# Optimization experiments

Measured on AMD Instinct MI355X. Metric: run time of the kernel, lower is better.

Reference implementation:

```python
import jax, jax.numpy as jnp
import numpy as np

B = 32
L = 256
NUM_AA = 20
LAMBDA_SINGLE = 1.0
LAMBDA_PAIR = 0.2 * (L - 1)


def setup_inputs() -> dict:
    key = jax.random.key(0)
    k1, k2, k3 = jax.random.split(key, 3)
    x = jax.random.randint(k1, (B, L), 0, NUM_AA, dtype=jnp.int32)
    # Embedding(num, 1) init: normal(0, embedding_dim**-0.5) = std 1.0
    w_single = jax.random.normal(k2, (L * NUM_AA, 1), dtype=jnp.float32)
    w_pair = jax.random.normal(k3, (L * L * NUM_AA * NUM_AA, 1), dtype=jnp.float32)
    return {"x": x, "w_single": w_single, "w_pair": w_pair}


def reference(x, w_single, w_pair):
    ws = w_single[:, 0]  # [L*20]
    wp = w_pair[:, 0]    # [L*L*400]
    Bn, Ln = x.shape
    pos = jnp.arange(Ln, dtype=jnp.int32)

    # singles[b, i] = ws[i*20 + x[b, i]]
    singles = ws[pos[None, :] * NUM_AA + x]  # [B, L]
    all_singles = jnp.broadcast_to(ws.reshape(Ln, NUM_AA), (Bn, Ln, NUM_AA))  # [B, L, 20]

    # pairs[b, i, j] = wp[(i*L + j)*400 + x[b,i]*20 + x[b,j]]
    idx_pairs = (pos[:, None] * Ln + pos[None, :]) * (NUM_AA * NUM_AA) \
        + x[:, :, None] * NUM_AA + x[:, None, :]  # [B, L, L]
    pairs = wp[idx_pairs]  # [B, L, L]

    # all_pairs reproduces the original in-place mutation semantics:
    # at outer iteration i (inner loop over j), x[:, p] has already been
    # overwritten to 19 for p < i, equals j for p == i, and is original for p > i.
    i_ax = pos[None, :, None, None]                      # [1, L, 1, 1]
    p_ax = pos[None, None, :, None]                      # [1, 1, L, 1]
    j_ax = jnp.arange(NUM_AA, dtype=jnp.int32)[None, None, None, :]  # [1,1,1,20]
    x_b = x[:, None, :, None]                            # [B, 1, L, 1]
    eff = jnp.where(p_ax < i_ax, NUM_AA - 1, jnp.where(p_ax == i_ax, j_ax, x_b))
    idx_all = (i_ax * Ln + p_ax) * (NUM_AA * NUM_AA) + j_ax * NUM_AA + eff  # [B,L,L,20]
    all_pairs = wp[idx_all]  # [B, L, L, 20]

    energy = singles + jnp.sum(pairs, axis=2)  # [B, L]
    logits = all_singles + jnp.sum(all_pairs, axis=2)  # [B, L, 20]
    total_energy = jax.nn.logsumexp(logits, axis=-1)  # [B, L]
    final_energy = jnp.mean(jnp.sum(-energy + total_energy, axis=1))

    single_reg = LAMBDA_SINGLE * jnp.sum(jnp.square(w_single))
    pair_reg = LAMBDA_PAIR * jnp.sum(jnp.square(w_pair))
    single_lasso = LAMBDA_SINGLE * jnp.sum(jnp.abs(w_single))
    pair_lasso = LAMBDA_PAIR * jnp.sum(jnp.abs(w_pair))
    return final_energy + single_reg + pair_reg + single_lasso + pair_lasso
```

## Files before the change

### kernel.cpp

```cpp
#include <hip/hip_runtime.h>
#include <cmath>

#define Bsz 32
#define Lsz 256
#define Asz 20
#define PAD 21
#define NCHUNK 4
#define PCH 64
#define GRP 8
#define NGRP (PCH/GRP)
#define BLK1 640

#define OFF_G 0
#define OFF_C (NCHUNK*Bsz*Lsz*Asz)
#define OFF_E (OFF_C + NCHUNK*Lsz*Asz)
#define OFF_RSQ (OFF_E + NCHUNK*Bsz*Lsz)
#define OFF_RAB (OFF_RSQ + Lsz*NCHUNK)
#define OFF_K2  (OFF_RAB + Lsz*NCHUNK)

__global__ __launch_bounds__(BLK1) void k1(const int* __restrict__ x,
                                           const float* __restrict__ wp,
                                           float* __restrict__ ws) {
  const int wg = blockIdx.x;
  const int c = wg & (NCHUNK - 1);
  const int i = wg >> 2;
  const int t = threadIdx.x;
  const int b = t / Asz;
  const int j = t - b * Asz;

  __shared__ float blk[GRP * Asz * PAD];
  __shared__ int   xs[Bsz * PCH];
  __shared__ int   xi[Bsz];
  __shared__ float red1[BLK1];
  __shared__ float red2[BLK1];

  const int pbase = c * PCH;
  for (int k = t; k < Bsz * PCH; k += BLK1) {
    int bb = k >> 6, pp = k & 63;
    xs[k] = x[bb * Lsz + pbase + pp];
  }
  if (t < Bsz) xi[t] = x[t * Lsz + i];
  __syncthreads();

  float accJ = 0.f;
  float accE = 0.f;
  float accC = 0.f;
  float rsq = 0.f, rab = 0.f;

  const float* wrow = wp + (size_t)(i * Lsz + pbase) * (Asz * Asz);

  float v0, v1, v2, v3, v4;
  {
    const float* g0 = wrow;
    v0 = g0[t]; v1 = g0[t + BLK1]; v2 = g0[t + 2*BLK1];
    v3 = g0[t + 3*BLK1]; v4 = g0[t + 4*BLK1];
  }

  for (int g = 0; g < NGRP; ++g) {
    {
      float vv[5] = {v0, v1, v2, v3, v4};
      #pragma unroll
      for (int k = 0; k < 5; ++k) {
        float v = vv[k];
        rsq += v * v;
        rab += fabsf(v);
        int o = k * BLK1 + t;
        int bi = o / 400;
        int w = o - bi * 400;
        int r = w / 20;
        int col = w - r * 20;
        blk[bi * (Asz * PAD) + r * PAD + col] = v;
      }
    }
    __syncthreads();

    if (g + 1 < NGRP) {
      const float* ns = wrow + (g + 1) * (GRP * 400);
      v0 = ns[t]; v1 = ns[t + BLK1]; v2 = ns[t + 2*BLK1];
      v3 = ns[t + 3*BLK1]; v4 = ns[t + 4*BLK1];
    }

    const int p0 = pbase + g * GRP;
    #pragma unroll
    for (int pp = 0; pp < GRP; ++pp) {
      const int p = p0 + pp;
      const float* bb = blk + pp * (Asz * PAD);
      const int xv = xs[b * PCH + (p - pbase)];
      if (p > i) accJ += bb[j * PAD + xv];
      if (j == 0) accE += bb[xi[b] * PAD + xv];
      if (t < Asz) {
        if (p < i)       accC += bb[t * PAD + 19];
        else if (p == i) accC += bb[t * PAD + t];
      }
    }
    __syncthreads();
  }

  ws[OFF_G + (((size_t)c * Bsz + b) * Lsz + i) * Asz + j] = accJ;
  if (j == 0) ws[OFF_E + (c * Bsz + b) * Lsz + i] = accE;
  if (t < Asz) ws[OFF_C + (c * Lsz + i) * Asz + t] = accC;

  red1[t] = rsq; red2[t] = rab;
  __syncthreads();
  for (int s = 320; s >= 5; s >>= 1) {
    if (t < s) { red1[t] += red1[t + s]; red2[t] += red2[t + s]; }
    __syncthreads();
  }
  if (t == 0) {
    ws[OFF_RSQ + wg] = red1[0] + red1[1] + red1[2] + red1[3] + red1[4];
    ws[OFF_RAB + wg] = red2[0] + red2[1] + red2[2] + red2[3] + red2[4];
  }
}

__global__ __launch_bounds__(256) void k2(const int* __restrict__ x,
                                          const float* __restrict__ wsingle,
                                          const float* __restrict__ ws,
                                          float* __restrict__ wso) {
  const int t = threadIdx.x;
  const int row = blockIdx.x * 256 + t;
  const int b = row >> 8;
  const int i = row & 255;

  float logits[Asz];
  float m = -1e30f;
  #pragma unroll
  for (int j = 0; j < Asz; ++j) {
    float v = wsingle[i * Asz + j];
    #pragma unroll
    for (int c = 0; c < NCHUNK; ++c) {
      v += ws[OFF_C + (c * Lsz + i) * Asz + j];
      v += ws[OFF_G + (((size_t)c * Bsz + b) * Lsz + i) * Asz + j];
    }
    logits[j] = v;
    m = fmaxf(m, v);
  }
  float se = 0.f;
  #pragma unroll
  for (int j = 0; j < Asz; ++j) se += expf(logits[j] - m);
  float lse = m + logf(se);

  float en = wsingle[i * Asz + x[b * Lsz + i]];
  #pragma unroll
  for (int c = 0; c < NCHUNK; ++c) en += ws[OFF_E + (c * Bsz + b) * Lsz + i];

  float val = lse - en;
  __shared__ float red[256];
  red[t] = val;
  __syncthreads();
  for (int s = 128; s >= 1; s >>= 1) {
    if (t < s) red[t] += red[t + s];
    __syncthreads();
  }
  if (t == 0) wso[OFF_K2 + blockIdx.x] = red[0];
}

__global__ __launch_bounds__(256) void k3(const float* __restrict__ wsingle,
                                          const float* __restrict__ ws,
                                          float* __restrict__ out) {
  const int t = threadIdx.x;
  float ssq = 0.f, sab = 0.f;
  for (int k = t; k < Lsz * Asz; k += 256) {
    float v = wsingle[k];
    ssq += v * v; sab += fabsf(v);
  }
  float psq = 0.f, pab = 0.f;
  for (int k = t; k < Lsz * NCHUNK; k += 256) {
    psq += ws[OFF_RSQ + k];
    pab += ws[OFF_RAB + k];
  }
  float fe = 0.f;
  if (t < 32) fe = ws[OFF_K2 + t];

  const float LP = (float)(0.2 * 255.0);
  float val = fe * (1.0f / Bsz) + (ssq + sab) + LP * (psq + pab);

  __shared__ float red[256];
  red[t] = val;
  __syncthreads();
  for (int s = 128; s >= 1; s >>= 1) {
    if (t < s) red[t] += red[t + s];
    __syncthreads();
  }
  if (t == 0) out[0] = red[0];
}

extern "C" void kernel_launch(void* const* d_in, const int* in_sizes, int n_in,
                              void* d_out, int out_size, void* d_ws, size_t ws_size,
                              hipStream_t stream) {
  const int*   x       = (const int*)d_in[0];
  const float* wsingle = (const float*)d_in[1];
  const float* wpair   = (const float*)d_in[2];
  float* ws  = (float*)d_ws;
  float* out = (float*)d_out;

  k1<<<Lsz * NCHUNK, BLK1, 0, stream>>>(x, wpair, ws);
  k2<<<(Bsz * Lsz) / 256, 256, 0, stream>>>(x, wsingle, ws, ws);
  k3<<<1, 256, 0, stream>>>(wsingle, ws, out);
}
```

Baseline: 180.2 us.

## Restructure pair kernel with float4 loads, finer chunks, skipped masked work, shuffle reductions

The pair-weight kernel now splits each row into 8 chunks of 32 positions, loads weights as float4 straight into unpadded shared memory, and uses a j-major thread mapping. Loop bounds skip positions where the mask leaves nothing to add. The energy, diagonal and column-19 terms move onto dedicated threads, and block reductions switch to wavefront shuffles. The logsumexp kernel is remapped to one block per position with fast exp/log, so the final kernel sums more partials. The unpadded layout may cause shared-memory bank conflicts, and doubling the chunks doubles the partial-result traffic.

```diff
diff --git a/kernel.cpp b/kernel.cpp
--- a/kernel.cpp
+++ b/kernel.cpp
@@ -4,174 +4,163 @@
 #define Bsz 32
 #define Lsz 256
 #define Asz 20
-#define PAD 21
-#define NCHUNK 4
-#define PCH 64
-#define GRP 8
-#define NGRP (PCH/GRP)
+#define NCHUNK 8
+#define PCH 32
+#define GRP 16
+#define NGRP 2
 #define BLK1 640
 
 #define OFF_G 0
-#define OFF_C (NCHUNK*Bsz*Lsz*Asz)
+#define OFF_C (NCHUNK*Lsz*Bsz*Asz)
 #define OFF_E (OFF_C + NCHUNK*Lsz*Asz)
-#define OFF_RSQ (OFF_E + NCHUNK*Bsz*Lsz)
-#define OFF_RAB (OFF_RSQ + Lsz*NCHUNK)
-#define OFF_K2  (OFF_RAB + Lsz*NCHUNK)
+#define OFF_RSQ (OFF_E + NCHUNK*Lsz*Bsz)
+#define OFF_RAB (OFF_RSQ + NCHUNK*Lsz)
+#define OFF_K2  (OFF_RAB + NCHUNK*Lsz)
 
-__global__ __launch_bounds__(BLK1) void k1(const int* __restrict__ x,
-                                           const float* __restrict__ wp,
-                                           float* __restrict__ ws) {
+__global__ __launch_bounds__(BLK1, 8) void k1(const int* __restrict__ x,
+                                              const float* __restrict__ wp,
+                                              float* __restrict__ ws) {
   const int wg = blockIdx.x;
   const int c = wg & (NCHUNK - 1);
-  const int i = wg >> 2;
+  const int i = wg >> 3;
   const int t = threadIdx.x;
-  const int b = t / Asz;
-  const int j = t - b * Asz;
+  const int j = t >> 5;
+  const int b = t & 31;
 
-  __shared__ float blk[GRP * Asz * PAD];
-  __shared__ int   xs[Bsz * PCH];
+  __shared__ float blk[GRP * 400];
+  __shared__ int   xs[PCH * Bsz];
   __shared__ int   xi[Bsz];
-  __shared__ float red1[BLK1];
-  __shared__ float red2[BLK1];
+  __shared__ float wred[32];
 
   const int pbase = c * PCH;
-  for (int k = t; k < Bsz * PCH; k += BLK1) {
-    int bb = k >> 6, pp = k & 63;
-    xs[k] = x[bb * Lsz + pbase + pp];
+  for (int k = t; k < PCH * Bsz; k += BLK1) {
+    int dp = k >> 5, bb = k & 31;
+    xs[k] = x[bb * Lsz + pbase + dp];
   }
   if (t < Bsz) xi[t] = x[t * Lsz + i];
-  __syncthreads();
 
-  float accJ = 0.f;
-  float accE = 0.f;
-  float accC = 0.f;
-  float rsq = 0.f, rab = 0.f;
+  float accJ = 0.f, accE = 0.f, accC = 0.f, rsq = 0.f, rab = 0.f;
 
-  const float* wrow = wp + (size_t)(i * Lsz + pbase) * (Asz * Asz);
-
-  float v0, v1, v2, v3, v4;
-  {
-    const float* g0 = wrow;
-    v0 = g0[t]; v1 = g0[t + BLK1]; v2 = g0[t + 2*BLK1];
-    v3 = g0[t + 3*BLK1]; v4 = g0[t + 4*BLK1];
-  }
+  const float4* wrow = (const float4*)(wp + (size_t)(i * Lsz + pbase) * 400);
+  float4 v0 = wrow[t];
+  float4 v1 = wrow[t + 640];
+  float4 v2 = (t < 320) ? wrow[t + 1280] : make_float4(0.f, 0.f, 0.f, 0.f);
 
   for (int g = 0; g < NGRP; ++g) {
-    {
-      float vv[5] = {v0, v1, v2, v3, v4};
-      #pragma unroll
-      for (int k = 0; k < 5; ++k) {
-        float v = vv[k];
-        rsq += v * v;
-        rab += fabsf(v);
-        int o = k * BLK1 + t;
-        int bi = o / 400;
-        int w = o - bi * 400;
-        int r = w / 20;
-        int col = w - r * 20;
-        blk[bi * (Asz * PAD) + r * PAD + col] = v;
-      }
+    float4* bf4 = (float4*)blk;
+    bf4[t] = v0;
+    bf4[t + 640] = v1;
+    if (t < 320) bf4[t + 1280] = v2;
+    rsq += v0.x*v0.x + v0.y*v0.y + v0.z*v0.z + v0.w*v0.w;
+    rsq += v1.x*v1.x + v1.y*v1.y + v1.z*v1.z + v1.w*v1.w;
+    rab += fabsf(v0.x)+fabsf(v0.y)+fabsf(v0.z)+fabsf(v0.w);
+    rab += fabsf(v1.x)+fabsf(v1.y)+fabsf(v1.z)+fabsf(v1.w);
+    if (t < 320) {
+      rsq += v2.x*v2.x + v2.y*v2.y + v2.z*v2.z + v2.w*v2.w;
+      rab += fabsf(v2.x)+fabsf(v2.y)+fabsf(v2.z)+fabsf(v2.w);
     }
     __syncthreads();
 
-    if (g + 1 < NGRP) {
-      const float* ns = wrow + (g + 1) * (GRP * 400);
-      v0 = ns[t]; v1 = ns[t + BLK1]; v2 = ns[t + 2*BLK1];
-      v3 = ns[t + 3*BLK1]; v4 = ns[t + 4*BLK1];
+    if (g == 0) {
+      v0 = wrow[1600 + t];
+      v1 = wrow[1600 + t + 640];
+      if (t < 320) v2 = wrow[1600 + t + 1280];
     }
 
     const int p0 = pbase + g * GRP;
-    #pragma unroll
-    for (int pp = 0; pp < GRP; ++pp) {
-      const int p = p0 + pp;
-      const float* bb = blk + pp * (Asz * PAD);
-      const int xv = xs[b * PCH + (p - pbase)];
-      if (p > i) accJ += bb[j * PAD + xv];
-      if (j == 0) accE += bb[xi[b] * PAD + xv];
-      if (t < Asz) {
-        if (p < i)       accC += bb[t * PAD + 19];
-        else if (p == i) accC += bb[t * PAD + t];
+    int ppstart = i + 1 - p0;
+    if (ppstart < 0) ppstart = 0;
+    const int jbase = j * Asz;
+    for (int pp = ppstart; pp < GRP; ++pp) {
+      int xv = xs[((g * GRP + pp) << 5) | b];
+      accJ += blk[pp * 400 + jbase + xv];
+    }
+    if (t < Bsz) {
+      const int ebase = xi[t] * Asz;
+      for (int pp = 0; pp < GRP; ++pp) {
+        int xv = xs[((g * GRP + pp) << 5) | t];
+        accE += blk[pp * 400 + ebase + xv];
       }
+    } else if (t < Bsz + Asz) {
+      const int jj = t - Bsz;
+      int pend = i - p0;
+      if (pend > GRP) pend = GRP;
+      for (int pp = 0; pp < pend; ++pp) accC += blk[pp * 400 + jj * Asz + 19];
+      const int pd = i - p0;
+      if (pd >= 0 && pd < GRP) accC += blk[pd * 400 + jj * Asz + jj];
     }
     __syncthreads();
   }
 
-  ws[OFF_G + (((size_t)c * Bsz + b) * Lsz + i) * Asz + j] = accJ;
-  if (j == 0) ws[OFF_E + (c * Bsz + b) * Lsz + i] = accE;
-  if (t < Asz) ws[OFF_C + (c * Lsz + i) * Asz + t] = accC;
+  ws[OFF_G + ((size_t)(c * Lsz + i) * Bsz + b) * Asz + j] = accJ;
+  if (t < Bsz) ws[OFF_E + (c * Lsz + i) * Bsz + t] = accE;
+  else if (t < Bsz + Asz) ws[OFF_C + (c * Lsz + i) * Asz + (t - Bsz)] = accC;
 
-  red1[t] = rsq; red2[t] = rab;
+  for (int s = 32; s >= 1; s >>= 1) {
+    rsq += __shfl_down(rsq, s);
+    rab += __shfl_down(rab, s);
+  }
+  if ((t & 63) == 0) { wred[t >> 6] = rsq; wred[16 + (t >> 6)] = rab; }
   __syncthreads();
-  for (int s = 320; s >= 5; s >>= 1) {
-    if (t < s) { red1[t] += red1[t + s]; red2[t] += red2[t + s]; }
-    __syncthreads();
-  }
   if (t == 0) {
-    ws[OFF_RSQ + wg] = red1[0] + red1[1] + red1[2] + red1[3] + red1[4];
-    ws[OFF_RAB + wg] = red2[0] + red2[1] + red2[2] + red2[3] + red2[4];
+    float a = 0.f, bb = 0.f;
+    for (int w = 0; w < 10; ++w) { a += wred[w]; bb += wred[16 + w]; }
+    ws[OFF_RSQ + wg] = a;
+    ws[OFF_RAB + wg] = bb;
   }
 }
 
-__global__ __launch_bounds__(256) void k2(const int* __restrict__ x,
-                                          const float* __restrict__ wsingle,
-                                          const float* __restrict__ ws,
-                                          float* __restrict__ wso) {
+__global__ __launch_bounds__(BLK1) void k2(const int* __restrict__ x,
+                                           const float* __restrict__ wsng,
+                                           const float* __restrict__ ws,
+                                           float* __restrict__ wso) {
+  const int i = blockIdx.x;
   const int t = threadIdx.x;
-  const int row = blockIdx.x * 256 + t;
-  const int b = row >> 8;
-  const int i = row & 255;
+  const int j = t >> 5, b = t & 31;
+  __shared__ float l[Bsz * 21];
 
-  float logits[Asz];
-  float m = -1e30f;
+  float v = wsng[i * Asz + j];
   #pragma unroll
-  for (int j = 0; j < Asz; ++j) {
-    float v = wsingle[i * Asz + j];
+  for (int c = 0; c < NCHUNK; ++c) {
+    v += ws[OFF_C + (c * Lsz + i) * Asz + j];
+    v += ws[OFF_G + ((size_t)(c * Lsz + i) * Bsz + b) * Asz + j];
+  }
+  l[b * 21 + j] = v;
+  __syncthreads();
+
+  if (t < Bsz) {
+    float m = -1e30f;
     #pragma unroll
-    for (int c = 0; c < NCHUNK; ++c) {
-      v += ws[OFF_C + (c * Lsz + i) * Asz + j];
-      v += ws[OFF_G + (((size_t)c * Bsz + b) * Lsz + i) * Asz + j];
-    }
-    logits[j] = v;
-    m = fmaxf(m, v);
+    for (int jj = 0; jj < Asz; ++jj) m = fmaxf(m, l[t * 21 + jj]);
+    float se = 0.f;
+    #pragma unroll
+    for (int jj = 0; jj < Asz; ++jj) se += __expf(l[t * 21 + jj] - m);
+    float lse = m + __logf(se);
+    float en = wsng[i * Asz + x[t * Lsz + i]];
+    #pragma unroll
+    for (int c = 0; c < NCHUNK; ++c) en += ws[OFF_E + (c * Lsz + i) * Bsz + t];
+    wso[OFF_K2 + i * Bsz + t] = lse - en;
   }
-  float se = 0.f;
-  #pragma unroll
-  for (int j = 0; j < Asz; ++j) se += expf(logits[j] - m);
-  float lse = m + logf(se);
-
-  float en = wsingle[i * Asz + x[b * Lsz + i]];
-  #pragma unroll
-  for (int c = 0; c < NCHUNK; ++c) en += ws[OFF_E + (c * Bsz + b) * Lsz + i];
-
-  float val = lse - en;
-  __shared__ float red[256];
-  red[t] = val;
-  __syncthreads();
-  for (int s = 128; s >= 1; s >>= 1) {
-    if (t < s) red[t] += red[t + s];
-    __syncthreads();
-  }
-  if (t == 0) wso[OFF_K2 + blockIdx.x] = red[0];
 }
 
-__global__ __launch_bounds__(256) void k3(const float* __restrict__ wsingle,
+__global__ __launch_bounds__(256) void k3(const float* __restrict__ wsng,
                                           const float* __restrict__ ws,
                                           float* __restrict__ out) {
   const int t = threadIdx.x;
   float ssq = 0.f, sab = 0.f;
   for (int k = t; k < Lsz * Asz; k += 256) {
-    float v = wsingle[k];
+    float v = wsng[k];
     ssq += v * v; sab += fabsf(v);
   }
   float psq = 0.f, pab = 0.f;
-  for (int k = t; k < Lsz * NCHUNK; k += 256) {
+  for (int k = t; k < NCHUNK * Lsz; k += 256) {
     psq += ws[OFF_RSQ + k];
     pab += ws[OFF_RAB + k];
   }
   float fe = 0.f;
-  if (t < 32) fe = ws[OFF_K2 + t];
+  for (int k = t; k < Lsz * Bsz; k += 256) fe += ws[OFF_K2 + k];
 
-  const float LP = (float)(0.2 * 255.0);
+  const float LP = 51.0f;
   float val = fe * (1.0f / Bsz) + (ssq + sab) + LP * (psq + pab);
 
   __shared__ float red[256];
@@ -194,6 +183,6 @@
   float* out = (float*)d_out;
 
   k1<<<Lsz * NCHUNK, BLK1, 0, stream>>>(x, wpair, ws);
-  k2<<<(Bsz * Lsz) / 256, 256, 0, stream>>>(x, wsingle, ws, ws);
+  k2<<<Lsz, BLK1, 0, stream>>>(x, wsingle, ws, ws);
   k3<<<1, 256, 0, stream>>>(wsingle, ws, out);
 }
```

Result: no change. 178.1 us (-1.2%).
